# Performance work log

Measured on AMD Instinct MI355X. Metric: run time of the kernel, lower is better.

The kernel has to match this reference:

```python
import jax, jax.numpy as jnp
import numpy as np

IN_F = 2
DIM_H = 64
DT = 0.02          # step_size
INTENSITY = 40.0   # Poisson rate multiplier
RATE = jnp.array([10.0, 1.0], dtype=jnp.float32)  # Gamma rates per feature


def _xavier(key, fan_in, fan_out):
    lim = float(np.sqrt(6.0 / (fan_in + fan_out)))
    return jax.random.uniform(key, (fan_in, fan_out), minval=-lim, maxval=lim, dtype=jnp.float32)


def setup_inputs() -> dict:
    key = jax.random.key(0)
    k0, k1, k2 = jax.random.split(key, 3)
    Nsim, steps = 100000, 200
    z0 = jax.random.normal(k0, (Nsim, IN_F), dtype=jnp.float32)
    W1 = _xavier(k1, IN_F, DIM_H)
    b1 = jnp.zeros((DIM_H,), dtype=jnp.float32)
    W2 = _xavier(k2, DIM_H, IN_F)
    b2 = jnp.zeros((IN_F,), dtype=jnp.float32)
    diffusion = jnp.float32(1.0)
    return {"z0": z0, "W1": W1, "b1": b1, "W2": W2, "b2": b2,
            "diffusion": diffusion, "Nsim": Nsim, "steps": steps}


def _drift(x, W1, b1, W2, b2):
    # MLP: Linear(2,64) -> tanh -> Linear(64,2)
    h = jnp.tanh(x @ W1 + b1)
    return h @ W2 + b2


def reference(z0, W1, b1, W2, b2, diffusion, Nsim, steps):
    sqrt_dt = jnp.float32(np.sqrt(DT))
    n = z0.shape[0]

    def step(state, key):
        kp, kn, kg = jax.random.split(key, 3)
        # Poisson(intensity*dt) jump counts, shape [N,1]
        pois = jax.random.poisson(kp, INTENSITY * DT, (n, 1)).astype(jnp.float32)
        a = jnp.broadcast_to(pois, (n, IN_F))  # Gamma concentration per feature
        # Gamma(conc=pois, rate=RATE); conc==0 -> sample is exactly 0
        g = jax.random.gamma(kg, jnp.maximum(a, 1.0), dtype=jnp.float32) / RATE
        jump = jnp.where(a > 0, g, 0.0)
        noise = jax.random.normal(kn, (n, IN_F), dtype=jnp.float32)
        new_state = (state
                     + _drift(state, W1, b1, W2, b2) * DT
                     + diffusion * sqrt_dt * noise
                     + jump)
        return new_state, new_state

    keys = jax.random.split(jax.random.key(42), steps)
    _, path = jax.lax.scan(step, z0, keys)            # [steps, N, F]
    path = jnp.concatenate([z0[None], path], axis=0)   # [steps+1, N, F]
    return jnp.transpose(path, (1, 0, 2))              # [N, steps+1, F]
```

## Files before the change

kernel.cpp:

```cpp
#include <hip/hip_runtime.h>
#include <cstdint>
#include <cmath>

#define DEVINL __device__ __forceinline__

struct U2 { uint32_t a, b; };

DEVINL uint32_t rotl32(uint32_t x, uint32_t r){ return (x << r) | (x >> (32u - r)); }

DEVINL U2 tf(uint32_t k0, uint32_t k1, uint32_t x0, uint32_t x1){
  const uint32_t k2 = k0 ^ k1 ^ 0x1BD11BDAu;
  x0 += k0; x1 += k1;
#define TFR(r) { x0 += x1; x1 = rotl32(x1,(r)); x1 ^= x0; }
  TFR(13) TFR(15) TFR(26) TFR(6)  x0 += k1; x1 += k2 + 1u;
  TFR(17) TFR(29) TFR(16) TFR(24) x0 += k2; x1 += k0 + 2u;
  TFR(13) TFR(15) TFR(26) TFR(6)  x0 += k0; x1 += k1 + 3u;
  TFR(17) TFR(29) TFR(16) TFR(24) x0 += k1; x1 += k2 + 4u;
  TFR(13) TFR(15) TFR(26) TFR(6)  x0 += k2; x1 += k0 + 5u;
#undef TFR
  U2 r; r.a = x0; r.b = x1; return r;
}

DEVINL uint32_t pbits(uint32_t k0, uint32_t k1, uint32_t idx){
  U2 r = tf(k0, k1, 0u, idx);
  return r.a ^ r.b;
}

DEVINL float u01(uint32_t bits){
  return __uint_as_float((bits >> 9) | 0x3F800000u) - 1.0f;
}

DEVINL float xla_logf(float xin){
  float xf = fmaxf(__uint_as_float(0x00800000u), xin);
  uint32_t ib = __float_as_uint(xf);
  float e = (float)((int)(ib >> 23) - 126);
  float x = __uint_as_float((ib & 0x807fffffu) | 0x3f000000u);
  bool m = x < 0.707106781186547524f;
  float t = m ? x : 0.0f;
  x = __fsub_rn(x, 1.0f);
  if (m) e = __fsub_rn(e, 1.0f);
  x = __fadd_rn(x, t);
  float z = __fmul_rn(x, x);
  float y = 7.0376836292e-2f;
  y = fmaf(y, x, -1.1514610310e-1f);
  y = fmaf(y, x,  1.1676998740e-1f);
  y = fmaf(y, x, -1.2420140846e-1f);
  y = fmaf(y, x,  1.4249322787e-1f);
  y = fmaf(y, x, -1.6668057665e-1f);
  y = fmaf(y, x,  2.0000714765e-1f);
  y = fmaf(y, x, -2.4999993993e-1f);
  y = fmaf(y, x,  3.3333331174e-1f);
  y = __fmul_rn(y, x);
  y = __fmul_rn(y, z);
  y = fmaf(e, -2.12194440e-4f, y);
  y = fmaf(z, -0.5f, y);
  x = __fadd_rn(x, y);
  x = fmaf(e, 0.693359375f, x);
  if (xin == 0.0f) x = __uint_as_float(0xff800000u);
  return x;
}

DEVINL float xla_log1pf(float v){
  float av = fabsf(v);
  if (av < 1e-4f) return __fmul_rn(__fadd_rn(__fmul_rn(-0.5f, v), 1.0f), v);
  return xla_logf(__fadd_rn(v, 1.0f));
}

DEVINL float erfinv32(float x){
  float xx = __fmul_rn(x, x);
  float w = -xla_log1pf(-xx);
  float p;
  if (w < 5.0f){
    float ww = __fsub_rn(w, 2.5f);
    p = 2.81022636e-08f;
    p = __fadd_rn( 3.43273939e-07f, __fmul_rn(p, ww));
    p = __fadd_rn(-3.5233877e-06f,  __fmul_rn(p, ww));
    p = __fadd_rn(-4.39150654e-06f, __fmul_rn(p, ww));
    p = __fadd_rn( 0.00021858087f,  __fmul_rn(p, ww));
    p = __fadd_rn(-0.00125372503f,  __fmul_rn(p, ww));
    p = __fadd_rn(-0.00417768164f,  __fmul_rn(p, ww));
    p = __fadd_rn( 0.246640727f,    __fmul_rn(p, ww));
    p = __fadd_rn( 1.50140941f,     __fmul_rn(p, ww));
  } else {
    float ww = __fsub_rn(sqrtf(w), 3.0f);
    p = -0.000200214257f;
    p = __fadd_rn( 0.000100950558f, __fmul_rn(p, ww));
    p = __fadd_rn( 0.00134934322f,  __fmul_rn(p, ww));
    p = __fadd_rn(-0.00367342844f,  __fmul_rn(p, ww));
    p = __fadd_rn( 0.00573950773f,  __fmul_rn(p, ww));
    p = __fadd_rn(-0.0076224613f,   __fmul_rn(p, ww));
    p = __fadd_rn( 0.00943887047f,  __fmul_rn(p, ww));
    p = __fadd_rn( 1.00167406f,     __fmul_rn(p, ww));
    p = __fadd_rn( 2.83297682f,     __fmul_rn(p, ww));
  }
  return __fmul_rn(p, x);
}

#define SQRT2F (__uint_as_float(0x3FB504F3u))
#define NLOF   (__uint_as_float(0xBF7FFFFFu))

DEVINL float normal_from_bits(uint32_t bits){
  float ff = u01(bits);
  float u = __fadd_rn(__fmul_rn(ff, 2.0f), NLOF);
  u = fmaxf(NLOF, u);
  return __fmul_rn(SQRT2F, erfinv32(u));
}

DEVINL float fast_tanh(float x){
  float ax = fabsf(x);
  float e = __expf(-2.0f * ax);
  float r = (1.0f - e) * __builtin_amdgcn_rcpf(1.0f + e);
  return __builtin_copysignf(r, x);
}

DEVINL float gamma_one(uint32_t gk0, uint32_t gk1, float alpha){
  const float d = __fsub_rn(alpha, (1.0f/3.0f));
  const float c = (1.0f/3.0f) / sqrtf(d);
  U2 K = tf(gk0, gk1, 0u, 0u);
  for (;;) {
    U2 xk = tf(K.a, K.b, 0u, 1u);
    U2 Uk = tf(K.a, K.b, 0u, 2u);
    float xx, v;
    for (;;) {
      U2 sub = tf(xk.a, xk.b, 0u, 1u);
      uint32_t nb = pbits(sub.a, sub.b, 0u);
      xx = normal_from_bits(nb);
      v = __fadd_rn(1.0f, __fmul_rn(xx, c));
      if (v > 0.0f) break;
      xk = tf(xk.a, xk.b, 0u, 0u);
    }
    float X = __fmul_rn(xx, xx);
    float V = __fmul_rn(__fmul_rn(v, v), v);
    float U = u01(pbits(Uk.a, Uk.b, 0u));
    float sq = __fsub_rn(1.0f, __fmul_rn(0.0331f, __fmul_rn(X, X)));
    if (U < sq) return __fmul_rn(d, V);
    float lnU = xla_logf(U);
    float lnV = xla_logf(V);
    float rhs = __fadd_rn(__fmul_rn(X, 0.5f),
                          __fmul_rn(d, __fadd_rn(__fsub_rn(1.0f, V), lnV)));
    if (lnU < rhs) return __fmul_rn(d, V);
    K = tf(K.a, K.b, 0u, 0u);
  }
}

#define NPK 24
#define WSTRIDE (4 + 2*NPK)
#define KEYOFF 8
#define JOFF   16384

__global__ void setup_kernel(uint32_t* __restrict__ ws, int steps){
  int t = blockIdx.x * blockDim.x + threadIdx.x;
  if (t >= steps) return;
  U2 kt = tf(0u, 42u, 0u, (uint32_t)t);
  U2 kp = tf(kt.a, kt.b, 0u, 0u);
  U2 kn = tf(kt.a, kt.b, 0u, 1u);
  U2 kg = tf(kt.a, kt.b, 0u, 2u);
  uint32_t* p = ws + KEYOFF + (size_t)t * WSTRIDE;
  p[0] = kn.a; p[1] = kn.b;
  p[2] = kg.a; p[3] = kg.b;
  uint32_t r0 = kp.a, r1 = kp.b;
  for (int i = 0; i < NPK; ++i) {
    U2 sub = tf(r0, r1, 0u, 1u);
    U2 rn  = tf(r0, r1, 0u, 0u);
    p[4 + 2*i] = sub.a; p[5 + 2*i] = sub.b;
    r0 = rn.a; r1 = rn.b;
  }
}

#define PEL 4
__global__ __launch_bounds__(64) void pois_kernel(
    uint32_t* __restrict__ ws, int N, int steps, uint32_t POFF, uint32_t COFF)
{
  const int lane = threadIdx.x;
  const int t = blockIdx.y;
  const int base = blockIdx.x * (64 * PEL);
  const uint32_t* __restrict__ p = ws + KEYOFF + (size_t)t * WSTRIDE;

  int poisv[PEL];
  #pragma unroll
  for (int j = 0; j < PEL; ++j) poisv[j] = -1;

  int cur = 0;
  int e = base + lane;
  float lp = 0.0f; int k = 0;
  bool done = (e >= N);

  #pragma unroll 1
  for (int guard = 0; guard < PEL * NPK + PEL + 1; ++guard) {
    if (!__any(!done)) break;
    if (!done) {
      if (!(lp > -0.8f)) {
        poisv[cur] = k - 1;
        cur++;
        lp = 0.0f; k = 0;
        int ne = base + cur * 64 + lane;
        if (cur >= PEL || ne >= N) done = true;
        else e = ne;
      }
    }
    if (!done) {
      uint32_t bits = pbits(p[4 + 2*k], p[5 + 2*k], (uint32_t)e);
      lp = __fadd_rn(lp, xla_logf(u01(bits)));
      k++;
      if (k >= NPK) lp = -1.0f;
    }
  }

  float* jarr = (float*)(ws + JOFF);
  uint8_t* pb = (uint8_t*)ws + (size_t)POFF * 4u + (size_t)t * (size_t)N;
  int mycnt = 0;
  #pragma unroll
  for (int j = 0; j < PEL; ++j) {
    int ej = base + j * 64 + lane;
    if (ej < N) {
      pb[ej] = (uint8_t)poisv[j];
      size_t jb = (size_t)t * (size_t)(2*N) + 2u * (uint32_t)ej;
      jarr[jb] = 0.0f; jarr[jb + 1] = 0.0f;
      if (poisv[j] > 0) mycnt++;
    }
  }
  int c = mycnt;
  #pragma unroll
  for (int off = 32; off > 0; off >>= 1) c += __shfl_xor(c, off, 64);
  if (lane == 0)
    ws[COFF + (size_t)t * gridDim.x + blockIdx.x] = (uint32_t)c;
}

__global__ __launch_bounds__(256) void prefix_kernel(
    uint32_t* __restrict__ ws, uint32_t COFF, uint32_t BOFF, int NB)
{
  __shared__ uint32_t ssum[256];
  int i = threadIdx.x;
  int chunk = (NB + 255) >> 8;
  int lo = i * chunk, hi = lo + chunk; if (hi > NB) hi = NB;
  uint32_t s = 0;
  for (int j = lo; j < hi; ++j) s += ws[COFF + j];
  ssum[i] = s;
  __syncthreads();
  if (i == 0) {
    uint32_t run = 0;
    for (int k = 0; k < 256; ++k) { uint32_t c = ssum[k]; ssum[k] = run; run += c; }
    ws[0] = run;
  }
  __syncthreads();
  uint32_t base = ssum[i];
  for (int j = lo; j < hi; ++j) { ws[BOFF + j] = base; base += ws[COFF + j]; }
}

__global__ __launch_bounds__(256) void scatter_kernel(
    uint32_t* __restrict__ ws, int N, int steps,
    uint32_t POFF, uint32_t BOFF, uint32_t WOFF, uint32_t CAP)
{
  __shared__ uint32_t cnts[4];
  int e = blockIdx.x * 256 + threadIdx.x;
  int t = blockIdx.y;
  bool act = e < N;
  uint32_t pv = 0;
  if (act) pv = ((const uint8_t*)ws)[(size_t)POFF*4u + (size_t)t*(size_t)N + (size_t)e];
  uint64_t b = __ballot(pv > 0);
  int lane = threadIdx.x & 63, w = threadIdx.x >> 6;
  if (lane == 0) cnts[w] = (uint32_t)__popcll(b);
  __syncthreads();
  uint32_t bid = (uint32_t)blockIdx.y * gridDim.x + blockIdx.x;
  uint32_t wb = ws[BOFF + bid];
  for (int w2 = 0; w2 < w; ++w2) wb += cnts[w2];
  if (pv > 0) {
    uint32_t rank = (uint32_t)__popcll(b & ((1ull << lane) - 1ull));
    uint32_t idx = wb + rank;
    if (idx < CAP)
      ws[WOFF + idx] = ((uint32_t)t << 23) | ((uint32_t)e << 6) | pv;
  }
}

__global__ __launch_bounds__(256) void gamma_kernel(
    uint32_t* __restrict__ ws, int N, uint32_t WOFF, uint32_t CAP)
{
  uint32_t total = ws[0]; if (total > CAP) total = CAP;
  uint32_t j = blockIdx.x * 256u + threadIdx.x;
  if (j >= 2u * total) return;
  uint32_t ent = ws[WOFF + (j >> 1)];
  uint32_t t = ent >> 23, e = (ent >> 6) & 0x1FFFFu, pv = ent & 0x3Fu;
  const uint32_t* __restrict__ p = ws + KEYOFF + (size_t)t * WSTRIDE;
  uint32_t f = j & 1u;
  U2 gk = tf(p[2], p[3], 0u, 2u*e + f);
  float s = gamma_one(gk.a, gk.b, (float)pv);
  float* jarr = (float*)(ws + JOFF);
  jarr[(size_t)t * (size_t)(2*N) + (size_t)(2u*e + f)] = f ? s : (s / 10.0f);
}

__global__ __launch_bounds__(256) void jump_kernel(
    uint32_t* __restrict__ ws, int N, int steps)
{
  int e = blockIdx.x * 256 + threadIdx.x;
  int t = blockIdx.y;
  if (e >= N) return;
  const uint32_t* __restrict__ p = ws + KEYOFF + (size_t)t * WSTRIDE;
  const uint32_t ue = (uint32_t)e;
  float lp = 0.0f; int k = 0;
  #pragma unroll 1
  for (int i = 0; i < NPK; ++i) {
    if (!(lp > -0.8f)) break;
    k++;
    uint32_t bits = pbits(p[4 + 2*i], p[5 + 2*i], ue);
    lp = __fadd_rn(lp, xla_logf(u01(bits)));
  }
  int pois = k - 1;
  float* jarr = (float*)(ws + JOFF);
  size_t jbase = (size_t)t * (size_t)(2*N) + (size_t)(2*e);
  float j0 = 0.0f, j1 = 0.0f;
  if (pois > 0) {
    uint32_t kg0 = p[2], kg1 = p[3];
    float alpha = (float)pois;
    U2 gk0 = tf(kg0, kg1, 0u, 2u*ue);
    j0 = gamma_one(gk0.a, gk0.b, alpha) / 10.0f;
    U2 gk1 = tf(kg0, kg1, 0u, 2u*ue + 1u);
    j1 = gamma_one(gk1.a, gk1.b, alpha);
  }
  jarr[jbase] = j0; jarr[jbase + 1] = j1;
}

#define IBLK 256
__global__ __launch_bounds__(IBLK) void integrate_kernel(
    const float* __restrict__ z0, const float* __restrict__ W1,
    const float* __restrict__ b1, const float* __restrict__ W2,
    const float* __restrict__ b2, const float* __restrict__ diffp,
    const uint32_t* __restrict__ ws, float* __restrict__ out,
    int N, int steps)
{
  __shared__ float smem[322];
  for (int k = threadIdx.x; k < 322; k += IBLK) {
    float v;
    if (k < 128)      v = W1[k];
    else if (k < 192) v = b1[k - 128];
    else if (k < 320) v = W2[k - 192];
    else              v = b2[k - 320];
    smem[k] = v;
  }
  __syncthreads();
  const float* sW1 = smem;
  const float* sb1 = smem + 128;
  const float* sW2 = smem + 192;
  const float* sb2 = smem + 320;

  int tid = blockIdx.x * IBLK + threadIdx.x;
  if (tid >= 2 * N) return;
  const int e = tid >> 1;
  const int f = tid & 1;
  const uint32_t utid = (uint32_t)tid;

  float x = z0[tid];
  const size_t obase = (size_t)e * (size_t)(steps + 1) * 2u + (size_t)f;
  out[obase] = x;

  const float DTf  = 0.02f;
  const float sqdt = (float)0.14142135623730951;
  const float coef = __fmul_rn(diffp[0], sqdt);
  const int   hbase = f << 5;
  const float* __restrict__ jarr = (const float*)(ws + JOFF);

  for (int t = 0; t < steps; ++t) {
    const uint32_t* __restrict__ p = ws + KEYOFF + (size_t)t * WSTRIDE;

    float jump = jarr[(size_t)t * (size_t)(2*N) + utid];

    float nf = normal_from_bits(pbits(p[0], p[1], utid));

    float xo = __shfl_xor(x, 1, 64);
    float xf0 = (f == 0) ? x : xo;
    float xf1 = (f == 0) ? xo : x;
    float p0 = 0.0f, p1 = 0.0f;
    #pragma unroll
    for (int i = 0; i < 32; ++i) {
      int h = hbase + i;
      float hv = fast_tanh(fmaf(xf0, sW1[h], fmaf(xf1, sW1[64 + h], sb1[h])));
      p0 = fmaf(hv, sW2[2*h],     p0);
      p1 = fmaf(hv, sW2[2*h + 1], p1);
    }
    float q0 = p0 + __shfl_xor(p0, 1, 64);
    float q1 = p1 + __shfl_xor(p1, 1, 64);
    float dr = sb2[f] + ((f == 0) ? q0 : q1);

    x = __fadd_rn(__fadd_rn(__fadd_rn(x, __fmul_rn(dr, DTf)),
                            __fmul_rn(coef, nf)), jump);
    out[obase + (size_t)(t + 1) * 2u] = x;
  }
}

__global__ __launch_bounds__(64) void sim_fallback_kernel(
    const float* __restrict__ z0, const float* __restrict__ W1,
    const float* __restrict__ b1, const float* __restrict__ W2,
    const float* __restrict__ b2, const float* __restrict__ diffp,
    const uint32_t* __restrict__ ws, float* __restrict__ out,
    int N, int steps)
{
  __shared__ float smem[322];
  for (int k = threadIdx.x; k < 322; k += 64) {
    float v;
    if (k < 128)      v = W1[k];
    else if (k < 192) v = b1[k - 128];
    else if (k < 320) v = W2[k - 192];
    else              v = b2[k - 320];
    smem[k] = v;
  }
  __syncthreads();
  const float* sW1 = smem;
  const float* sb1 = smem + 128;
  const float* sW2 = smem + 192;
  const float* sb2 = smem + 320;

  int tid = blockIdx.x * 64 + threadIdx.x;
  if (tid >= 2 * N) return;
  const int e = tid >> 1;
  const int f = tid & 1;
  const uint32_t ue   = (uint32_t)e;
  const uint32_t utid = (uint32_t)tid;

  float x = z0[tid];
  const size_t obase = (size_t)e * (size_t)(steps + 1) * 2u + (size_t)f;
  out[obase] = x;

  const float DTf  = 0.02f;
  const float sqdt = (float)0.14142135623730951;
  const float coef = __fmul_rn(diffp[0], sqdt);
  const int   hbase = f << 5;

  for (int t = 0; t < steps; ++t) {
    const uint32_t* __restrict__ p = ws + KEYOFF + (size_t)t * WSTRIDE;
    int pois;
    {
      float lp = 0.0f;
      pois = NPK - 1;
      #pragma unroll 1
      for (int m = 0; m < NPK/2; ++m) {
        int i0 = 2*m + f;
        uint32_t bits = pbits(p[4 + 2*i0], p[5 + 2*i0], ue);
        float lmine = xla_logf(u01(bits));
        float lother = __shfl_xor(lmine, 1, 64);
        float la = (f == 0) ? lmine : lother;
        float lb = (f == 0) ? lother : lmine;
        float s1 = __fadd_rn(lp, la);
        float s2 = __fadd_rn(s1, lb);
        if (!(s1 > -0.8f)) { pois = 2*m; break; }
        if (!(s2 > -0.8f)) { pois = 2*m + 1; break; }
        lp = s2;
      }
    }
    float nf = normal_from_bits(pbits(p[0], p[1], utid));
    float jump = 0.0f;
    if (pois > 0) {
      U2 gk = tf(p[2], p[3], 0u, utid);
      float s = gamma_one(gk.a, gk.b, (float)pois);
      jump = (f == 0) ? (s / 10.0f) : s;
    }
    float xo = __shfl_xor(x, 1, 64);
    float xf0 = (f == 0) ? x : xo;
    float xf1 = (f == 0) ? xo : x;
    float p0 = 0.0f, p1 = 0.0f;
    #pragma unroll
    for (int i = 0; i < 32; ++i) {
      int h = hbase + i;
      float hv = fast_tanh(fmaf(xf0, sW1[h], fmaf(xf1, sW1[64 + h], sb1[h])));
      p0 = fmaf(hv, sW2[2*h],     p0);
      p1 = fmaf(hv, sW2[2*h + 1], p1);
    }
    float q0 = p0 + __shfl_xor(p0, 1, 64);
    float q1 = p1 + __shfl_xor(p1, 1, 64);
    float dr = sb2[f] + ((f == 0) ? q0 : q1);
    x = __fadd_rn(__fadd_rn(__fadd_rn(x, __fmul_rn(dr, DTf)),
                            __fmul_rn(coef, nf)), jump);
    out[obase + (size_t)(t + 1) * 2u] = x;
  }
}

extern "C" void kernel_launch(void* const* d_in, const int* in_sizes, int n_in,
                              void* d_out, int out_size, void* d_ws, size_t ws_size,
                              hipStream_t stream) {
  const float* z0  = (const float*)d_in[0];
  const float* W1  = (const float*)d_in[1];
  const float* b1  = (const float*)d_in[2];
  const float* W2  = (const float*)d_in[3];
  const float* b2  = (const float*)d_in[4];
  const float* dif = (const float*)d_in[5];
  int N = in_sizes[0] / 2;
  int steps = out_size / (N * 2) - 1;
  uint32_t* ws = (uint32_t*)d_ws;
  int total = 2 * N;

  hipLaunchKernelGGL(setup_kernel, dim3((steps + 255) / 256), dim3(256), 0, stream,
                     ws, steps);

  size_t JSZ = (size_t)2 * (size_t)N * (size_t)steps;
  size_t PSZ = ((size_t)N * (size_t)steps + 3u) / 4u;
  int    NBX = (N + 255) / 256;
  size_t NB  = (size_t)NBX * (size_t)steps;
  size_t CAP = ((size_t)N * (size_t)steps * 11u) / 16u;
  size_t POFFs = (size_t)JOFF + JSZ;
  size_t COFFs = POFFs + PSZ;
  size_t BOFFs = COFFs + NB;
  size_t WOFFs = BOFFs + NB;
  size_t need0 = (WOFFs + CAP) * 4u;
  size_t need1 = ((size_t)JOFF + JSZ) * 4u;
  bool pk = (N < (1 << 17)) && (steps < (1 << 9)) && (steps <= 314) &&
            (WOFFs + CAP < 0xFFFFFFFFull);

  if (pk && ws_size >= need0) {
    hipLaunchKernelGGL(pois_kernel, dim3(NBX, steps), dim3(64), 0, stream,
                       ws, N, steps, (uint32_t)POFFs, (uint32_t)COFFs);
    hipLaunchKernelGGL(prefix_kernel, dim3(1), dim3(256), 0, stream,
                       ws, (uint32_t)COFFs, (uint32_t)BOFFs, (int)NB);
    hipLaunchKernelGGL(scatter_kernel, dim3(NBX, steps), dim3(256), 0, stream,
                       ws, N, steps, (uint32_t)POFFs, (uint32_t)BOFFs,
                       (uint32_t)WOFFs, (uint32_t)CAP);
    size_t gth = 2u * CAP;
    hipLaunchKernelGGL(gamma_kernel, dim3((gth + 255) / 256), dim3(256), 0, stream,
                       ws, N, (uint32_t)WOFFs, (uint32_t)CAP);
    hipLaunchKernelGGL(integrate_kernel, dim3((total + IBLK - 1) / IBLK), dim3(IBLK),
                       0, stream, z0, W1, b1, W2, b2, dif, ws, (float*)d_out, N, steps);
  } else if (steps <= 314 && ws_size >= need1) {
    hipLaunchKernelGGL(jump_kernel, dim3((N + 255) / 256, steps), dim3(256), 0, stream,
                       ws, N, steps);
    hipLaunchKernelGGL(integrate_kernel, dim3((total + IBLK - 1) / IBLK), dim3(IBLK),
                       0, stream, z0, W1, b1, W2, b2, dif, ws, (float*)d_out, N, steps);
  } else {
    hipLaunchKernelGGL(sim_fallback_kernel, dim3((total + 63) / 64), dim3(64), 0, stream,
                       z0, W1, b1, W2, b2, dif, ws, (float*)d_out, N, steps);
  }
}
```

Before: 1.729 ms.

## Precompute Brownian noise in jump kernels and vectorize integrate MLP with packed FMA

```diff
diff --git a/kernel.cpp b/kernel.cpp
--- a/kernel.cpp
+++ b/kernel.cpp
@@ -5,6 +5,7 @@
 #define DEVINL __device__ __forceinline__
 
 struct U2 { uint32_t a, b; };
+typedef float v2f __attribute__((ext_vector_type(2)));
 
 DEVINL uint32_t rotl32(uint32_t x, uint32_t r){ return (x << r) | (x >> (32u - r)); }
 
@@ -98,6 +99,7 @@
 
 #define SQRT2F (__uint_as_float(0x3FB504F3u))
 #define NLOF   (__uint_as_float(0xBF7FFFFFu))
+#define SQDTF  ((float)0.14142135623730951)
 
 DEVINL float normal_from_bits(uint32_t bits){
   float ff = u01(bits);
@@ -112,6 +114,8 @@
   float r = (1.0f - e) * __builtin_amdgcn_rcpf(1.0f + e);
   return __builtin_copysignf(r, x);
 }
+
+DEVINL v2f f2fma(v2f a, v2f b, v2f c){ return __builtin_elementwise_fma(a, b, c); }
 
 DEVINL float gamma_one(uint32_t gk0, uint32_t gk1, float alpha){
   const float d = __fsub_rn(alpha, (1.0f/3.0f));
@@ -169,12 +173,14 @@
 
 #define PEL 4
 __global__ __launch_bounds__(64) void pois_kernel(
-    uint32_t* __restrict__ ws, int N, int steps, uint32_t POFF, uint32_t COFF)
+    uint32_t* __restrict__ ws, const float* __restrict__ diffp,
+    int N, int steps, uint32_t POFF, uint32_t COFF)
 {
   const int lane = threadIdx.x;
   const int t = blockIdx.y;
   const int base = blockIdx.x * (64 * PEL);
   const uint32_t* __restrict__ p = ws + KEYOFF + (size_t)t * WSTRIDE;
+  const float coef = __fmul_rn(diffp[0], SQDTF);
 
   int poisv[PEL];
   #pragma unroll
@@ -208,14 +214,18 @@
 
   float* jarr = (float*)(ws + JOFF);
   uint8_t* pb = (uint8_t*)ws + (size_t)POFF * 4u + (size_t)t * (size_t)N;
+  const uint32_t kn0 = p[0], kn1 = p[1];
   int mycnt = 0;
   #pragma unroll
   for (int j = 0; j < PEL; ++j) {
     int ej = base + j * 64 + lane;
     if (ej < N) {
       pb[ej] = (uint8_t)poisv[j];
+      float nf0 = normal_from_bits(pbits(kn0, kn1, 2u*(uint32_t)ej));
+      float nf1 = normal_from_bits(pbits(kn0, kn1, 2u*(uint32_t)ej + 1u));
       size_t jb = (size_t)t * (size_t)(2*N) + 2u * (uint32_t)ej;
-      jarr[jb] = 0.0f; jarr[jb + 1] = 0.0f;
+      jarr[jb]     = __fmul_rn(coef, nf0);
+      jarr[jb + 1] = __fmul_rn(coef, nf1);
       if (poisv[j] > 0) mycnt++;
     }
   }
@@ -284,18 +294,21 @@
   uint32_t f = j & 1u;
   U2 gk = tf(p[2], p[3], 0u, 2u*e + f);
   float s = gamma_one(gk.a, gk.b, (float)pv);
+  float jv = f ? s : (s / 10.0f);
   float* jarr = (float*)(ws + JOFF);
-  jarr[(size_t)t * (size_t)(2*N) + (size_t)(2u*e + f)] = f ? s : (s / 10.0f);
+  float* slot = &jarr[(size_t)t * (size_t)(2*N) + (size_t)(2u*e + f)];
+  *slot = __fadd_rn(*slot, jv);
 }
 
 __global__ __launch_bounds__(256) void jump_kernel(
-    uint32_t* __restrict__ ws, int N, int steps)
+    uint32_t* __restrict__ ws, const float* __restrict__ diffp, int N, int steps)
 {
   int e = blockIdx.x * 256 + threadIdx.x;
   int t = blockIdx.y;
   if (e >= N) return;
   const uint32_t* __restrict__ p = ws + KEYOFF + (size_t)t * WSTRIDE;
   const uint32_t ue = (uint32_t)e;
+  const float coef = __fmul_rn(diffp[0], SQDTF);
   float lp = 0.0f; int k = 0;
   #pragma unroll 1
   for (int i = 0; i < NPK; ++i) {
@@ -305,17 +318,19 @@
     lp = __fadd_rn(lp, xla_logf(u01(bits)));
   }
   int pois = k - 1;
-  float* jarr = (float*)(ws + JOFF);
-  size_t jbase = (size_t)t * (size_t)(2*N) + (size_t)(2*e);
-  float j0 = 0.0f, j1 = 0.0f;
+  float nf0 = normal_from_bits(pbits(p[0], p[1], 2u*ue));
+  float nf1 = normal_from_bits(pbits(p[0], p[1], 2u*ue + 1u));
+  float j0 = __fmul_rn(coef, nf0), j1 = __fmul_rn(coef, nf1);
   if (pois > 0) {
     uint32_t kg0 = p[2], kg1 = p[3];
     float alpha = (float)pois;
     U2 gk0 = tf(kg0, kg1, 0u, 2u*ue);
-    j0 = gamma_one(gk0.a, gk0.b, alpha) / 10.0f;
+    j0 = __fadd_rn(j0, gamma_one(gk0.a, gk0.b, alpha) / 10.0f);
     U2 gk1 = tf(kg0, kg1, 0u, 2u*ue + 1u);
-    j1 = gamma_one(gk1.a, gk1.b, alpha);
-  }
+    j1 = __fadd_rn(j1, gamma_one(gk1.a, gk1.b, alpha));
+  }
+  float* jarr = (float*)(ws + JOFF);
+  size_t jbase = (size_t)t * (size_t)(2*N) + (size_t)(2*e);
   jarr[jbase] = j0; jarr[jbase + 1] = j1;
 }
 
@@ -353,35 +368,37 @@
   out[obase] = x;
 
   const float DTf  = 0.02f;
-  const float sqdt = (float)0.14142135623730951;
-  const float coef = __fmul_rn(diffp[0], sqdt);
   const int   hbase = f << 5;
   const float* __restrict__ jarr = (const float*)(ws + JOFF);
 
   for (int t = 0; t < steps; ++t) {
-    const uint32_t* __restrict__ p = ws + KEYOFF + (size_t)t * WSTRIDE;
-
-    float jump = jarr[(size_t)t * (size_t)(2*N) + utid];
-
-    float nf = normal_from_bits(pbits(p[0], p[1], utid));
+    float S = jarr[(size_t)t * (size_t)(2*N) + utid];
 
     float xo = __shfl_xor(x, 1, 64);
     float xf0 = (f == 0) ? x : xo;
     float xf1 = (f == 0) ? xo : x;
-    float p0 = 0.0f, p1 = 0.0f;
+    v2f xv0 = (v2f){xf0, xf0};
+    v2f xv1 = (v2f){xf1, xf1};
+    v2f acc = (v2f){0.0f, 0.0f};
     #pragma unroll
-    for (int i = 0; i < 32; ++i) {
-      int h = hbase + i;
-      float hv = fast_tanh(fmaf(xf0, sW1[h], fmaf(xf1, sW1[64 + h], sb1[h])));
-      p0 = fmaf(hv, sW2[2*h],     p0);
-      p1 = fmaf(hv, sW2[2*h + 1], p1);
-    }
-    float q0 = p0 + __shfl_xor(p0, 1, 64);
-    float q1 = p1 + __shfl_xor(p1, 1, 64);
+    for (int j = 0; j < 16; ++j) {
+      int h = hbase + 2*j;
+      v2f w1lo = *(const v2f*)&sW1[h];
+      v2f w1hi = *(const v2f*)&sW1[64 + h];
+      v2f b1v  = *(const v2f*)&sb1[h];
+      v2f pre  = f2fma(xv0, w1lo, f2fma(xv1, w1hi, b1v));
+      float hv0 = fast_tanh(pre.x);
+      float hv1 = fast_tanh(pre.y);
+      v2f w2a = *(const v2f*)&sW2[2*h];
+      v2f w2b = *(const v2f*)&sW2[2*h + 2];
+      acc = f2fma((v2f){hv0, hv0}, w2a, acc);
+      acc = f2fma((v2f){hv1, hv1}, w2b, acc);
+    }
+    float q0 = acc.x + __shfl_xor(acc.x, 1, 64);
+    float q1 = acc.y + __shfl_xor(acc.y, 1, 64);
     float dr = sb2[f] + ((f == 0) ? q0 : q1);
 
-    x = __fadd_rn(__fadd_rn(__fadd_rn(x, __fmul_rn(dr, DTf)),
-                            __fmul_rn(coef, nf)), jump);
+    x = __fadd_rn(__fadd_rn(x, __fmul_rn(dr, DTf)), S);
     out[obase + (size_t)(t + 1) * 2u] = x;
   }
 }
@@ -420,8 +437,7 @@
   out[obase] = x;
 
   const float DTf  = 0.02f;
-  const float sqdt = (float)0.14142135623730951;
-  const float coef = __fmul_rn(diffp[0], sqdt);
+  const float coef = __fmul_rn(diffp[0], SQDTF);
   const int   hbase = f << 5;
 
   for (int t = 0; t < steps; ++t) {
@@ -505,7 +521,7 @@
 
   if (pk && ws_size >= need0) {
     hipLaunchKernelGGL(pois_kernel, dim3(NBX, steps), dim3(64), 0, stream,
-                       ws, N, steps, (uint32_t)POFFs, (uint32_t)COFFs);
+                       ws, dif, N, steps, (uint32_t)POFFs, (uint32_t)COFFs);
     hipLaunchKernelGGL(prefix_kernel, dim3(1), dim3(256), 0, stream,
                        ws, (uint32_t)COFFs, (uint32_t)BOFFs, (int)NB);
     hipLaunchKernelGGL(scatter_kernel, dim3(NBX, steps), dim3(256), 0, stream,
@@ -518,7 +534,7 @@
                        0, stream, z0, W1, b1, W2, b2, dif, ws, (float*)d_out, N, steps);
   } else if (steps <= 314 && ws_size >= need1) {
     hipLaunchKernelGGL(jump_kernel, dim3((N + 255) / 256, steps), dim3(256), 0, stream,
-                       ws, N, steps);
+                       ws, dif, N, steps);
     hipLaunchKernelGGL(integrate_kernel, dim3((total + IBLK - 1) / IBLK), dim3(IBLK),
                        0, stream, z0, W1, b1, W2, b2, dif, ws, (float*)d_out, N, steps);
   } else {
```

Measured after the change: 1.594 ms. 1.08x faster.
